# Kernel optimization log

Hardware: AMD Instinct MI355X
Metric: run time of the kernel (lower is better)

## Reference

```python
import jax, jax.numpy as jnp
import numpy as np

INPUT_DIM = 57
D_MODEL = 64
D_STATE = 16
D_CONV = 4
EXPAND = 2
N_LAYERS = 2
OUT_SIZE = 6
D_INNER = EXPAND * D_MODEL            # 128
DT_RANK = (D_MODEL + 15) // 16        # 4
BATCH, SEQ = 4, 4096


def setup_inputs() -> dict:
    key = jax.random.key(0)
    ks = jax.random.split(key, 12)
    s = 0.02
    nl = N_LAYERS
    x = jax.random.normal(ks[0], (BATCH, SEQ, INPUT_DIM), jnp.float32)
    w_in = jax.random.normal(ks[1], (D_MODEL, INPUT_DIM), jnp.float32) * s
    b_in = jnp.zeros((D_MODEL,), jnp.float32)
    in_proj_w = jax.random.normal(ks[2], (nl, 2 * D_INNER, D_MODEL), jnp.float32) * s
    conv_w = jax.random.normal(ks[3], (nl, D_INNER, 1, D_CONV), jnp.float32) * 0.2
    conv_b = jnp.zeros((nl, D_INNER), jnp.float32)
    x_proj_w = jax.random.normal(ks[4], (nl, DT_RANK + 2 * D_STATE, D_INNER), jnp.float32) * s
    dt_proj_w = jax.random.normal(ks[5], (nl, D_INNER, DT_RANK), jnp.float32) * 0.1
    dt_proj_b = jax.random.normal(ks[6], (nl, D_INNER), jnp.float32) * 0.1
    # S4D-real init: A[d, n] = n+1  ->  A_log = log(1..d_state)
    A_log = jnp.log(jnp.broadcast_to(
        jnp.arange(1, D_STATE + 1, dtype=jnp.float32)[None, None, :],
        (nl, D_INNER, D_STATE)))
    D_skip = jnp.ones((nl, D_INNER), jnp.float32)
    out_proj_w = jax.random.normal(ks[7], (nl, D_MODEL, D_INNER), jnp.float32) * s
    w_cls = jax.random.normal(ks[8], (OUT_SIZE, D_MODEL), jnp.float32) * s
    b_cls = jnp.zeros((OUT_SIZE,), jnp.float32)
    return {"x": x, "w_in": w_in, "b_in": b_in, "in_proj_w": in_proj_w,
            "conv_w": conv_w, "conv_b": conv_b, "x_proj_w": x_proj_w,
            "dt_proj_w": dt_proj_w, "dt_proj_b": dt_proj_b, "A_log": A_log,
            "D_skip": D_skip, "out_proj_w": out_proj_w,
            "w_cls": w_cls, "b_cls": b_cls}


def _mamba_block(h, ipw, cw, cb, xpw, dpw, dpb, Alog, Dp, opw):
    B, L, _ = h.shape
    xz = h @ ipw.T                                  # (B, L, 2*D_INNER)
    xp, z = jnp.split(xz, 2, axis=-1)
    # depthwise causal conv over time
    xc = jnp.transpose(xp, (0, 2, 1))               # (B, D_INNER, L)
    xc = jax.lax.conv_general_dilated(
        xc, cw, window_strides=(1,), padding=[(D_CONV - 1, 0)],
        dimension_numbers=("NCH", "OIH", "NCH"),
        feature_group_count=D_INNER) + cb[None, :, None]
    u = jax.nn.silu(jnp.transpose(xc, (0, 2, 1)))   # (B, L, D_INNER)
    dbl = u @ xpw.T                                 # (B, L, DT_RANK + 2*D_STATE)
    dt, Bm, Cm = jnp.split(dbl, [DT_RANK, DT_RANK + D_STATE], axis=-1)
    delta = jax.nn.softplus(dt @ dpw.T + dpb)       # (B, L, D_INNER)
    A = -jnp.exp(Alog)                              # (D_INNER, D_STATE)

    def step(hst, inp):
        u_t, d_t, B_t, C_t = inp                    # (B,Di), (B,Di), (B,N), (B,N)
        hst = jnp.exp(d_t[:, :, None] * A) * hst + \
              (d_t * u_t)[:, :, None] * B_t[:, None, :]
        y_t = jnp.einsum("bdn,bn->bd", hst, C_t)
        return hst, y_t

    h0 = jnp.zeros((B, D_INNER, D_STATE), h.dtype)
    xs = (jnp.swapaxes(u, 0, 1), jnp.swapaxes(delta, 0, 1),
          jnp.swapaxes(Bm, 0, 1), jnp.swapaxes(Cm, 0, 1))
    _, ys = jax.lax.scan(step, h0, xs)              # (L, B, D_INNER)
    y = jnp.swapaxes(ys, 0, 1) + u * Dp
    y = y * jax.nn.silu(z)
    return y @ opw.T                                # (B, L, D_MODEL)


def reference(x, w_in, b_in, in_proj_w, conv_w, conv_b, x_proj_w,
              dt_proj_w, dt_proj_b, A_log, D_skip, out_proj_w, w_cls, b_cls):
    h = x @ w_in.T + b_in                           # linear_in
    for i in range(N_LAYERS):                       # residual mamba blocks
        h = h + _mamba_block(h, in_proj_w[i], conv_w[i], conv_b[i],
                             x_proj_w[i], dt_proj_w[i], dt_proj_b[i],
                             A_log[i], D_skip[i], out_proj_w[i])
    pooled = jnp.mean(h, axis=1)                    # AdaptiveAvgPool1d(1)
    return pooled @ w_cls.T + b_cls
```

## Files before the change

kernel.cpp:

```cpp
#include <hip/hip_runtime.h>


#define NB 4
#define SL 4096
#define NC 256
#define CT 16

__device__ __forceinline__ float siluf(float x) { return x / (1.f + __expf(-x)); }
__device__ __forceinline__ float softplusf(float x) { return x > 20.f ? x : log1pf(__expf(x)); }

__global__ __launch_bounds__(256) void k_prep(const float* __restrict__ opw, float* __restrict__ opwT) {
  int i = blockIdx.x * 256 + threadIdx.x;
  int l = i >> 13;
  int rem = i & 8191;
  int d = rem >> 6, m = rem & 63;
  opwT[i] = opw[l * 8192 + m * 128 + d];
}

__global__ __launch_bounds__(256) void k_linin(const float* __restrict__ x, const float* __restrict__ w,
                                               const float* __restrict__ bias, float* __restrict__ h) {
  __shared__ __align__(16) float xs[64][60];
  __shared__ __align__(16) float ws[64][60];
  const int t = threadIdx.x;
  const int r0 = blockIdx.x * 64;
  for (int i = t; i < 64 * 57; i += 256) {
    int r = i / 57, k = i - r * 57;
    xs[r][k] = x[(r0 + r) * 57 + k];
    ws[r][k] = w[i];
  }
  for (int i = t; i < 64 * 3; i += 256) {
    int r = i / 3, j = i - r * 3;
    xs[r][57 + j] = 0.f;
    ws[r][57 + j] = 0.f;
  }
  __syncthreads();
  const int col = t & 63;
  const int rg = t >> 6;
  float wreg[15][4];
#pragma unroll
  for (int k4 = 0; k4 < 15; ++k4) {
    float4 v = *(const float4*)&ws[col][k4 * 4];
    wreg[k4][0] = v.x; wreg[k4][1] = v.y; wreg[k4][2] = v.z; wreg[k4][3] = v.w;
  }
  const float bcol = bias[col];
  for (int g = 0; g < 4; ++g) {
    const int rb = rg * 16 + g * 4;
    float acc[4] = {bcol, bcol, bcol, bcol};
#pragma unroll
    for (int k4 = 0; k4 < 15; ++k4) {
#pragma unroll
      for (int i = 0; i < 4; ++i) {
        float4 xv = *(const float4*)&xs[rb + i][k4 * 4];
        acc[i] = fmaf(xv.x, wreg[k4][0], acc[i]);
        acc[i] = fmaf(xv.y, wreg[k4][1], acc[i]);
        acc[i] = fmaf(xv.z, wreg[k4][2], acc[i]);
        acc[i] = fmaf(xv.w, wreg[k4][3], acc[i]);
      }
    }
#pragma unroll
    for (int i = 0; i < 4; ++i) h[(r0 + rb + i) * 64 + col] = acc[i];
  }
}

__global__ __launch_bounds__(256) void k_inproj(const float* __restrict__ hin, const float* __restrict__ W,
                                                float* __restrict__ xp, float* __restrict__ z) {
  __shared__ __align__(16) float ht[64][68];
  __shared__ __align__(16) float wt[64][68];
  const int t = threadIdx.x;
  const int r0 = blockIdx.x * 64;
  const int c0 = blockIdx.y * 64;
  for (int idx = t; idx < 64 * 16; idx += 256) {
    int r = idx >> 4, k4 = idx & 15;
    float4 v = *(const float4*)(hin + (r0 + r) * 64 + 4 * k4);
    ht[4 * k4 + 0][r] = v.x; ht[4 * k4 + 1][r] = v.y; ht[4 * k4 + 2][r] = v.z; ht[4 * k4 + 3][r] = v.w;
  }
  for (int idx = t; idx < 64 * 16; idx += 256) {
    int c = idx >> 4, k4 = idx & 15;
    float4 v = *(const float4*)(W + (c0 + c) * 64 + 4 * k4);
    wt[4 * k4 + 0][c] = v.x; wt[4 * k4 + 1][c] = v.y; wt[4 * k4 + 2][c] = v.z; wt[4 * k4 + 3][c] = v.w;
  }
  __syncthreads();
  const int tc = t & 15, tr = t >> 4;
  float acc[4][4] = {};
  for (int k = 0; k < 64; ++k) {
    float4 a = *(const float4*)&ht[k][4 * tr];
    float4 b = *(const float4*)&wt[k][4 * tc];
    float av[4] = {a.x, a.y, a.z, a.w};
    float bv[4] = {b.x, b.y, b.z, b.w};
#pragma unroll
    for (int i = 0; i < 4; ++i)
#pragma unroll
      for (int j = 0; j < 4; ++j) acc[i][j] = fmaf(av[i], bv[j], acc[i][j]);
  }
#pragma unroll
  for (int i = 0; i < 4; ++i) {
    int row = r0 + 4 * tr + i;
    int c = c0 + 4 * tc;
    float4 v = make_float4(acc[i][0], acc[i][1], acc[i][2], acc[i][3]);
    if (c0 < 128) *(float4*)(xp + row * 128 + c) = v;
    else          *(float4*)(z + row * 128 + (c - 128)) = v;
  }
}

__global__ __launch_bounds__(256, 4) void k_mid(const float* __restrict__ xp, const float* __restrict__ cw,
                                                const float* __restrict__ cb, const float* __restrict__ xpw,
                                                const float* __restrict__ dpw, const float* __restrict__ dpb,
                                                const float* __restrict__ Alog,
                                                float* __restrict__ u_g, float* __restrict__ dl_g,
                                                float* __restrict__ B_g, float* __restrict__ C_g,
                                                float* __restrict__ chP, float* __restrict__ chH) {
  __shared__ __align__(16) float ush[16][132];
  __shared__ __align__(16) float dsh[16][132];
  __shared__ __align__(16) float wsh[36][132];
  __shared__ __align__(16) float dbl[16][40];

  const int t = threadIdx.x;
  const int c = blockIdx.x;
  const int b = blockIdx.y;
  const int grow0 = b * SL + c * CT;

  for (int i = t; i < 36 * 128; i += 256) {
    int cc = i >> 7, dd = i & 127;
    wsh[cc][dd] = xpw[cc * 128 + dd];
  }
  for (int i = t; i < 16 * 128; i += 256) {
    int r = i >> 7, dd = i & 127;
    float4 cwv = *(const float4*)(cw + dd * 4);
    const float* base = xp + (size_t)(grow0 + r) * 128 + dd;
    int l = c * CT + r;
    float acc = cb[dd] + base[0] * cwv.w;
    if (l >= 1) acc += base[-128] * cwv.z;
    if (l >= 2) acc += base[-256] * cwv.y;
    if (l >= 3) acc += base[-384] * cwv.x;
    float uu = siluf(acc);
    ush[r][dd] = uu;
    u_g[(size_t)(grow0 + r) * 128 + dd] = uu;
  }
  __syncthreads();

  if (t < 144) {
    int r = t / 9, cg = t - (t / 9) * 9;
    int cc = cg * 4;
    float a0 = 0, a1 = 0, a2 = 0, a3 = 0;
#pragma unroll 8
    for (int k4 = 0; k4 < 32; ++k4) {
      float4 uu = *(const float4*)&ush[r][4 * k4];
      float4 w0 = *(const float4*)&wsh[cc + 0][4 * k4];
      float4 w1 = *(const float4*)&wsh[cc + 1][4 * k4];
      float4 w2 = *(const float4*)&wsh[cc + 2][4 * k4];
      float4 w3 = *(const float4*)&wsh[cc + 3][4 * k4];
      a0 += uu.x * w0.x + uu.y * w0.y + uu.z * w0.z + uu.w * w0.w;
      a1 += uu.x * w1.x + uu.y * w1.y + uu.z * w1.z + uu.w * w1.w;
      a2 += uu.x * w2.x + uu.y * w2.y + uu.z * w2.z + uu.w * w2.w;
      a3 += uu.x * w3.x + uu.y * w3.y + uu.z * w3.z + uu.w * w3.w;
    }
    dbl[r][cc + 0] = a0; dbl[r][cc + 1] = a1; dbl[r][cc + 2] = a2; dbl[r][cc + 3] = a3;
  }
  __syncthreads();

  for (int i = t; i < 16 * 128; i += 256) {
    int r = i >> 7, dd = i & 127;
    float4 wv = *(const float4*)(dpw + dd * 4);
    float acc = dpb[dd] + dbl[r][0] * wv.x + dbl[r][1] * wv.y + dbl[r][2] * wv.z + dbl[r][3] * wv.w;
    float dt = softplusf(acc);
    dsh[r][dd] = dt;
    dl_g[(size_t)(grow0 + r) * 128 + dd] = dt;
  }
  for (int i = t; i < 16 * 32; i += 256) {
    int r = i >> 5, j = i & 31;
    float v = dbl[r][4 + j];
    if (j < 16) B_g[(grow0 + r) * 16 + j] = v;
    else        C_g[(grow0 + r) * 16 + (j - 16)] = v;
  }
  __syncthreads();

  {
    const int d = t & 127, hf = t >> 7, n0 = hf * 8;
    float a[8], hst[8];
#pragma unroll
    for (int j = 0; j < 8; ++j) {
      a[j] = -__expf(Alog[d * 16 + n0 + j]);
      hst[j] = 0.f;
    }
    float dts = 0.f;
#pragma unroll 4
    for (int tt = 0; tt < CT; ++tt) {
      float dt = dsh[tt][d];
      float du = dt * ush[tt][d];
      dts += dt;
#pragma unroll
      for (int j = 0; j < 8; ++j) {
        float e = __expf(dt * a[j]);
        hst[j] = fmaf(e, hst[j], du * dbl[tt][4 + n0 + j]);
      }
    }
    int off = ((b * 128 + d) * NC + c) * 16 + n0;
    float p[8];
#pragma unroll
    for (int j = 0; j < 8; ++j) p[j] = __expf(dts * a[j]);
    *(float4*)(chP + off + 0) = make_float4(p[0], p[1], p[2], p[3]);
    *(float4*)(chP + off + 4) = make_float4(p[4], p[5], p[6], p[7]);
    *(float4*)(chH + off + 0) = make_float4(hst[0], hst[1], hst[2], hst[3]);
    *(float4*)(chH + off + 4) = make_float4(hst[4], hst[5], hst[6], hst[7]);
  }
}

__global__ __launch_bounds__(256) void k_scan2p(const float* __restrict__ chP, float* chH) {
  __shared__ float sP[16][16];
  __shared__ float sH[16][16];
  const int t = threadIdx.x;
  const int n = t & 15, g = t >> 4;
  const int d = blockIdx.x, b = blockIdx.y;
  const int base = ((b * 128 + d) * NC) * 16 + n;

  float Pl[16], Hl[16];
  float cp = 1.f, ch = 0.f;
#pragma unroll
  for (int i = 0; i < 16; ++i) {
    int idx = base + (g * 16 + i) * 16;
    float P = chP[idx];
    float H = chH[idx];
    Pl[i] = P; Hl[i] = H;
    ch = fmaf(P, ch, H);
    cp *= P;
  }
  sP[g][n] = cp; sH[g][n] = ch;
  __syncthreads();
#pragma unroll
  for (int s = 1; s < 16; s <<= 1) {
    float pL = 1.f, hL = 0.f;
    if (g >= s) { pL = sP[g - s][n]; hL = sH[g - s][n]; }
    __syncthreads();
    ch = fmaf(cp, hL, ch);
    cp = cp * pL;
    sP[g][n] = cp; sH[g][n] = ch;
    __syncthreads();
  }
  float carry = 0.f;
  if (g > 0) carry = sH[g - 1][n];
#pragma unroll
  for (int i = 0; i < 16; ++i) {
    int idx = base + (g * 16 + i) * 16;
    chH[idx] = carry;
    carry = fmaf(Pl[i], carry, Hl[i]);
  }
}

__global__ __launch_bounds__(256, 5) void k_back(const float* __restrict__ u_g, const float* __restrict__ dl_g,
                                                 const float* __restrict__ B_g, const float* __restrict__ C_g,
                                                 const float* __restrict__ z_g, const float* __restrict__ cin,
                                                 const float* __restrict__ Alog, const float* __restrict__ Dsk,
                                                 const float* __restrict__ opwT, float* __restrict__ h) {
  __shared__ __align__(16) float ush[16][132];
  __shared__ __align__(16) float dsh[16][132];
  __shared__ float bsh[16][16];
  __shared__ float csh[16][16];
  __shared__ __align__(16) float ygsh[128][20];

  const int t = threadIdx.x;
  const int c = blockIdx.x;
  const int b = blockIdx.y;
  const int grow0 = b * SL + c * CT;

  for (int i = t; i < 16 * 128; i += 256) {
    int r = i >> 7, dd = i & 127;
    ush[r][dd] = u_g[(size_t)(grow0 + r) * 128 + dd];
    dsh[r][dd] = dl_g[(size_t)(grow0 + r) * 128 + dd];
  }
  for (int i = t; i < 16 * 32; i += 256) {
    int r = i >> 5, j = i & 31;
    if (j < 16) bsh[r][j] = B_g[(grow0 + r) * 16 + j];
    else        csh[r][j - 16] = C_g[(grow0 + r) * 16 + (j - 16)];
  }
  __syncthreads();

  {
    const int d = t >> 1, hf = t & 1, n0 = hf * 8;
    float a[8], hst[8];
    size_t off = ((size_t)(b * 128 + d) * NC + c) * 16 + n0;
    float4 h0 = *(const float4*)(cin + off + 0);
    float4 h1 = *(const float4*)(cin + off + 4);
    hst[0] = h0.x; hst[1] = h0.y; hst[2] = h0.z; hst[3] = h0.w;
    hst[4] = h1.x; hst[5] = h1.y; hst[6] = h1.z; hst[7] = h1.w;
#pragma unroll
    for (int j = 0; j < 8; ++j) a[j] = -__expf(Alog[d * 16 + n0 + j]);
    const float Dd = Dsk[d];
#pragma unroll 4
    for (int tt = 0; tt < CT; ++tt) {
      float dt = dsh[tt][d];
      float ut = ush[tt][d];
      float du = dt * ut;
      float yv = 0.f;
#pragma unroll
      for (int j = 0; j < 8; ++j) {
        float e = __expf(dt * a[j]);
        hst[j] = fmaf(e, hst[j], du * bsh[tt][n0 + j]);
        yv = fmaf(hst[j], csh[tt][n0 + j], yv);
      }
      float tot = yv + __shfl_xor(yv, 1);
      if (hf == 0) {
        float y = tot + ut * Dd;
        float zv = z_g[(size_t)(grow0 + tt) * 128 + d];
        ygsh[d][tt] = y * siluf(zv);
      }
    }
  }
  __syncthreads();

  {
    const int o = t & 63, q = t >> 6;
    float acc0 = 0.f, acc1 = 0.f, acc2 = 0.f, acc3 = 0.f;
#pragma unroll 8
    for (int k = 0; k < 128; ++k) {
      float w = opwT[k * 64 + o];
      float4 yv = *(const float4*)&ygsh[k][q * 4];
      acc0 = fmaf(yv.x, w, acc0);
      acc1 = fmaf(yv.y, w, acc1);
      acc2 = fmaf(yv.z, w, acc2);
      acc3 = fmaf(yv.w, w, acc3);
    }
    h[(size_t)(grow0 + q * 4 + 0) * 64 + o] += acc0;
    h[(size_t)(grow0 + q * 4 + 1) * 64 + o] += acc1;
    h[(size_t)(grow0 + q * 4 + 2) * 64 + o] += acc2;
    h[(size_t)(grow0 + q * 4 + 3) * 64 + o] += acc3;
  }
}

__global__ __launch_bounds__(256) void k_poolpart(const float* __restrict__ h, float* __restrict__ pp) {
  const int lb = blockIdx.x;
  const int b = blockIdx.y;
  const int t = threadIdx.x;
  const int d = t & 63, part = t >> 6;
  float s = 0.f;
  for (int i = 0; i < 32; ++i) {
    int l = lb * 128 + part + i * 4;
    s += h[(size_t)(b * SL + l) * 64 + d];
  }
  __shared__ float red[256];
  red[t] = s;
  __syncthreads();
  if (t < 64) pp[(b * 32 + lb) * 64 + t] = red[t] + red[t + 64] + red[t + 128] + red[t + 192];
}

__global__ __launch_bounds__(256) void k_cls(const float* __restrict__ pp, const float* __restrict__ wc,
                                             const float* __restrict__ bc, float* __restrict__ out) {
  const int t = threadIdx.x;
  __shared__ float pooled[4][64];
  int b = t >> 6, d = t & 63;
  float s = 0.f;
  for (int lb = 0; lb < 32; ++lb) s += pp[(b * 32 + lb) * 64 + d];
  pooled[b][d] = s * (1.f / 4096.f);
  __syncthreads();
  if (t < 24) {
    int bb = t / 6, o = t - bb * 6;
    float acc = bc[o];
    for (int d2 = 0; d2 < 64; ++d2) acc += pooled[bb][d2] * wc[o * 64 + d2];
    out[bb * 6 + o] = acc;
  }
}

extern "C" void kernel_launch(void* const* d_in, const int* in_sizes, int n_in,
                              void* d_out, int out_size, void* d_ws, size_t ws_size,
                              hipStream_t stream) {
  const float* x    = (const float*)d_in[0];
  const float* w_in = (const float*)d_in[1];
  const float* b_in = (const float*)d_in[2];
  const float* ipw  = (const float*)d_in[3];
  const float* cw   = (const float*)d_in[4];
  const float* cb   = (const float*)d_in[5];
  const float* xpw  = (const float*)d_in[6];
  const float* dpw  = (const float*)d_in[7];
  const float* dpb  = (const float*)d_in[8];
  const float* Alog = (const float*)d_in[9];
  const float* Dsk  = (const float*)d_in[10];
  const float* opw  = (const float*)d_in[11];
  const float* wc   = (const float*)d_in[12];
  const float* bc   = (const float*)d_in[13];
  float* out = (float*)d_out;

  float* ws   = (float*)d_ws;
  float* h    = ws;
  float* xp   = h + 1048576;
  float* zb   = xp + 2097152;
  float* ub   = zb + 2097152;
  float* dl   = ub + 2097152;
  float* Bb   = dl + 2097152;
  float* Cb   = Bb + 262144;
  float* chP  = Cb + 262144;
  float* chH  = chP + 2097152;
  float* opwT = chH + 2097152;
  float* pp   = opwT + 16384;

  k_prep<<<64, 256, 0, stream>>>(opw, opwT);
  k_linin<<<256, 256, 0, stream>>>(x, w_in, b_in, h);
  for (int i = 0; i < 2; ++i) {
    k_inproj<<<dim3(256, 4), 256, 0, stream>>>(h, ipw + i * 16384, xp, zb);
    k_mid<<<dim3(NC, 4), 256, 0, stream>>>(xp, cw + i * 512, cb + i * 128,
                                           xpw + i * 4608, dpw + i * 512, dpb + i * 128,
                                           Alog + i * 2048, ub, dl, Bb, Cb, chP, chH);
    k_scan2p<<<dim3(128, 4), 256, 0, stream>>>(chP, chH);
    k_back<<<dim3(NC, 4), 256, 0, stream>>>(ub, dl, Bb, Cb, zb, chH,
                                            Alog + i * 2048, Dsk + i * 128,
                                            opwT + i * 8192, h);
  }
  k_poolpart<<<dim3(32, 4), 256, 0, stream>>>(h, pp);
  k_cls<<<1, 256, 0, stream>>>(pp, wc, bc, out);
}
```

Measured before the change: 246.7 us.

## Drop chunk decay buffer, fuse pooling into back kernel, remove prep kernels

k_mid now stores only the per-chunk dt sum instead of the full 16-state decay products. The scan kernel recomputes the decays from dt sum and A, and the chunk-state layout changes to chunk-major. Pooling moves into k_back through atomics on the last layer, which removes the poolpart kernel and the out_proj transpose prep kernel. The x_proj weights are read straight from global memory instead of being staged in LDS, and k_mid's occupancy hint is raised to 6. Atomics make the pooled sum order nondeterministic, and the scan's strided reads of dt sums may be less coalesced.

```diff
diff --git a/kernel.cpp b/kernel.cpp
--- a/kernel.cpp
+++ b/kernel.cpp
@@ -9,20 +9,14 @@
 __device__ __forceinline__ float siluf(float x) { return x / (1.f + __expf(-x)); }
 __device__ __forceinline__ float softplusf(float x) { return x > 20.f ? x : log1pf(__expf(x)); }
 
-__global__ __launch_bounds__(256) void k_prep(const float* __restrict__ opw, float* __restrict__ opwT) {
-  int i = blockIdx.x * 256 + threadIdx.x;
-  int l = i >> 13;
-  int rem = i & 8191;
-  int d = rem >> 6, m = rem & 63;
-  opwT[i] = opw[l * 8192 + m * 128 + d];
-}
-
 __global__ __launch_bounds__(256) void k_linin(const float* __restrict__ x, const float* __restrict__ w,
-                                               const float* __restrict__ bias, float* __restrict__ h) {
+                                               const float* __restrict__ bias, float* __restrict__ h,
+                                               float* __restrict__ pool) {
   __shared__ __align__(16) float xs[64][60];
   __shared__ __align__(16) float ws[64][60];
   const int t = threadIdx.x;
   const int r0 = blockIdx.x * 64;
+  if (blockIdx.x == 0) pool[t] = 0.f;
   for (int i = t; i < 64 * 57; i += 256) {
     int r = i / 57, k = i - r * 57;
     xs[r][k] = x[(r0 + r) * 57 + k];
@@ -102,16 +96,15 @@
   }
 }
 
-__global__ __launch_bounds__(256, 4) void k_mid(const float* __restrict__ xp, const float* __restrict__ cw,
+__global__ __launch_bounds__(256, 6) void k_mid(const float* __restrict__ xp, const float* __restrict__ cw,
                                                 const float* __restrict__ cb, const float* __restrict__ xpw,
                                                 const float* __restrict__ dpw, const float* __restrict__ dpb,
                                                 const float* __restrict__ Alog,
                                                 float* __restrict__ u_g, float* __restrict__ dl_g,
                                                 float* __restrict__ B_g, float* __restrict__ C_g,
-                                                float* __restrict__ chP, float* __restrict__ chH) {
+                                                float* __restrict__ chH, float* __restrict__ dtsumG) {
   __shared__ __align__(16) float ush[16][132];
   __shared__ __align__(16) float dsh[16][132];
-  __shared__ __align__(16) float wsh[36][132];
   __shared__ __align__(16) float dbl[16][40];
 
   const int t = threadIdx.x;
@@ -119,10 +112,6 @@
   const int b = blockIdx.y;
   const int grow0 = b * SL + c * CT;
 
-  for (int i = t; i < 36 * 128; i += 256) {
-    int cc = i >> 7, dd = i & 127;
-    wsh[cc][dd] = xpw[cc * 128 + dd];
-  }
   for (int i = t; i < 16 * 128; i += 256) {
     int r = i >> 7, dd = i & 127;
     float4 cwv = *(const float4*)(cw + dd * 4);
@@ -141,18 +130,19 @@
   if (t < 144) {
     int r = t / 9, cg = t - (t / 9) * 9;
     int cc = cg * 4;
+    const float4* w0 = (const float4*)(xpw + (cc + 0) * 128);
+    const float4* w1 = (const float4*)(xpw + (cc + 1) * 128);
+    const float4* w2 = (const float4*)(xpw + (cc + 2) * 128);
+    const float4* w3 = (const float4*)(xpw + (cc + 3) * 128);
     float a0 = 0, a1 = 0, a2 = 0, a3 = 0;
 #pragma unroll 8
     for (int k4 = 0; k4 < 32; ++k4) {
       float4 uu = *(const float4*)&ush[r][4 * k4];
-      float4 w0 = *(const float4*)&wsh[cc + 0][4 * k4];
-      float4 w1 = *(const float4*)&wsh[cc + 1][4 * k4];
-      float4 w2 = *(const float4*)&wsh[cc + 2][4 * k4];
-      float4 w3 = *(const float4*)&wsh[cc + 3][4 * k4];
-      a0 += uu.x * w0.x + uu.y * w0.y + uu.z * w0.z + uu.w * w0.w;
-      a1 += uu.x * w1.x + uu.y * w1.y + uu.z * w1.z + uu.w * w1.w;
-      a2 += uu.x * w2.x + uu.y * w2.y + uu.z * w2.z + uu.w * w2.w;
-      a3 += uu.x * w3.x + uu.y * w3.y + uu.z * w3.z + uu.w * w3.w;
+      float4 v0 = w0[k4], v1 = w1[k4], v2 = w2[k4], v3 = w3[k4];
+      a0 += uu.x * v0.x + uu.y * v0.y + uu.z * v0.z + uu.w * v0.w;
+      a1 += uu.x * v1.x + uu.y * v1.y + uu.z * v1.z + uu.w * v1.w;
+      a2 += uu.x * v2.x + uu.y * v2.y + uu.z * v2.z + uu.w * v2.w;
+      a3 += uu.x * v3.x + uu.y * v3.y + uu.z * v3.z + uu.w * v3.w;
     }
     dbl[r][cc + 0] = a0; dbl[r][cc + 1] = a1; dbl[r][cc + 2] = a2; dbl[r][cc + 3] = a3;
   }
@@ -194,35 +184,33 @@
         hst[j] = fmaf(e, hst[j], du * dbl[tt][4 + n0 + j]);
       }
     }
-    int off = ((b * 128 + d) * NC + c) * 16 + n0;
-    float p[8];
-#pragma unroll
-    for (int j = 0; j < 8; ++j) p[j] = __expf(dts * a[j]);
-    *(float4*)(chP + off + 0) = make_float4(p[0], p[1], p[2], p[3]);
-    *(float4*)(chP + off + 4) = make_float4(p[4], p[5], p[6], p[7]);
+    size_t off = ((size_t)(b * NC + c) * 128 + d) * 16 + n0;
     *(float4*)(chH + off + 0) = make_float4(hst[0], hst[1], hst[2], hst[3]);
     *(float4*)(chH + off + 4) = make_float4(hst[4], hst[5], hst[6], hst[7]);
-  }
-}
-
-__global__ __launch_bounds__(256) void k_scan2p(const float* __restrict__ chP, float* chH) {
+    if (hf == 0) dtsumG[(b * NC + c) * 128 + d] = dts;
+  }
+}
+
+__global__ __launch_bounds__(256) void k_scan2p(const float* __restrict__ Alog,
+                                                const float* __restrict__ dtsumG, float* chH) {
   __shared__ float sP[16][16];
   __shared__ float sH[16][16];
   const int t = threadIdx.x;
   const int n = t & 15, g = t >> 4;
   const int d = blockIdx.x, b = blockIdx.y;
-  const int base = ((b * 128 + d) * NC) * 16 + n;
-
-  float Pl[16], Hl[16];
+  const float A2 = -__expf(Alog[d * 16 + n]);
+
+  float el[16], Hl[16];
   float cp = 1.f, ch = 0.f;
 #pragma unroll
   for (int i = 0; i < 16; ++i) {
-    int idx = base + (g * 16 + i) * 16;
-    float P = chP[idx];
-    float H = chH[idx];
-    Pl[i] = P; Hl[i] = H;
-    ch = fmaf(P, ch, H);
-    cp *= P;
+    int cc = g * 16 + i;
+    float ds = dtsumG[(b * NC + cc) * 128 + d];
+    float e = __expf(ds * A2);
+    float H = chH[((size_t)(b * NC + cc) * 128 + d) * 16 + n];
+    el[i] = e; Hl[i] = H;
+    ch = fmaf(e, ch, H);
+    cp *= e;
   }
   sP[g][n] = cp; sH[g][n] = ch;
   __syncthreads();
@@ -240,9 +228,9 @@
   if (g > 0) carry = sH[g - 1][n];
 #pragma unroll
   for (int i = 0; i < 16; ++i) {
-    int idx = base + (g * 16 + i) * 16;
+    size_t idx = ((size_t)(b * NC + g * 16 + i) * 128 + d) * 16 + n;
     chH[idx] = carry;
-    carry = fmaf(Pl[i], carry, Hl[i]);
+    carry = fmaf(el[i], carry, Hl[i]);
   }
 }
 
@@ -250,7 +238,8 @@
                                                  const float* __restrict__ B_g, const float* __restrict__ C_g,
                                                  const float* __restrict__ z_g, const float* __restrict__ cin,
                                                  const float* __restrict__ Alog, const float* __restrict__ Dsk,
-                                                 const float* __restrict__ opwT, float* __restrict__ h) {
+                                                 const float* __restrict__ opw, float* __restrict__ h,
+                                                 float* __restrict__ pool, int doPool) {
   __shared__ __align__(16) float ush[16][132];
   __shared__ __align__(16) float dsh[16][132];
   __shared__ float bsh[16][16];
@@ -277,7 +266,7 @@
   {
     const int d = t >> 1, hf = t & 1, n0 = hf * 8;
     float a[8], hst[8];
-    size_t off = ((size_t)(b * 128 + d) * NC + c) * 16 + n0;
+    size_t off = ((size_t)(b * NC + c) * 128 + d) * 16 + n0;
     float4 h0 = *(const float4*)(cin + off + 0);
     float4 h1 = *(const float4*)(cin + off + 4);
     hst[0] = h0.x; hst[1] = h0.y; hst[2] = h0.z; hst[3] = h0.w;
@@ -311,51 +300,40 @@
     const int o = t & 63, q = t >> 6;
     float acc0 = 0.f, acc1 = 0.f, acc2 = 0.f, acc3 = 0.f;
 #pragma unroll 8
-    for (int k = 0; k < 128; ++k) {
-      float w = opwT[k * 64 + o];
-      float4 yv = *(const float4*)&ygsh[k][q * 4];
-      acc0 = fmaf(yv.x, w, acc0);
-      acc1 = fmaf(yv.y, w, acc1);
-      acc2 = fmaf(yv.z, w, acc2);
-      acc3 = fmaf(yv.w, w, acc3);
-    }
-    h[(size_t)(grow0 + q * 4 + 0) * 64 + o] += acc0;
-    h[(size_t)(grow0 + q * 4 + 1) * 64 + o] += acc1;
-    h[(size_t)(grow0 + q * 4 + 2) * 64 + o] += acc2;
-    h[(size_t)(grow0 + q * 4 + 3) * 64 + o] += acc3;
-  }
-}
-
-__global__ __launch_bounds__(256) void k_poolpart(const float* __restrict__ h, float* __restrict__ pp) {
-  const int lb = blockIdx.x;
-  const int b = blockIdx.y;
-  const int t = threadIdx.x;
-  const int d = t & 63, part = t >> 6;
-  float s = 0.f;
-  for (int i = 0; i < 32; ++i) {
-    int l = lb * 128 + part + i * 4;
-    s += h[(size_t)(b * SL + l) * 64 + d];
-  }
-  __shared__ float red[256];
-  red[t] = s;
-  __syncthreads();
-  if (t < 64) pp[(b * 32 + lb) * 64 + t] = red[t] + red[t + 64] + red[t + 128] + red[t + 192];
-}
-
-__global__ __launch_bounds__(256) void k_cls(const float* __restrict__ pp, const float* __restrict__ wc,
-                                             const float* __restrict__ bc, float* __restrict__ out) {
-  const int t = threadIdx.x;
-  __shared__ float pooled[4][64];
-  int b = t >> 6, d = t & 63;
-  float s = 0.f;
-  for (int lb = 0; lb < 32; ++lb) s += pp[(b * 32 + lb) * 64 + d];
-  pooled[b][d] = s * (1.f / 4096.f);
-  __syncthreads();
+    for (int k4 = 0; k4 < 32; ++k4) {
+      float4 w4 = *(const float4*)(opw + o * 128 + 4 * k4);
+      float4 y0 = *(const float4*)&ygsh[4 * k4 + 0][q * 4];
+      float4 y1 = *(const float4*)&ygsh[4 * k4 + 1][q * 4];
+      float4 y2 = *(const float4*)&ygsh[4 * k4 + 2][q * 4];
+      float4 y3 = *(const float4*)&ygsh[4 * k4 + 3][q * 4];
+      acc0 = fmaf(y0.x, w4.x, acc0); acc0 = fmaf(y1.x, w4.y, acc0);
+      acc0 = fmaf(y2.x, w4.z, acc0); acc0 = fmaf(y3.x, w4.w, acc0);
+      acc1 = fmaf(y0.y, w4.x, acc1); acc1 = fmaf(y1.y, w4.y, acc1);
+      acc1 = fmaf(y2.y, w4.z, acc1); acc1 = fmaf(y3.y, w4.w, acc1);
+      acc2 = fmaf(y0.z, w4.x, acc2); acc2 = fmaf(y1.z, w4.y, acc2);
+      acc2 = fmaf(y2.z, w4.z, acc2); acc2 = fmaf(y3.z, w4.w, acc2);
+      acc3 = fmaf(y0.w, w4.x, acc3); acc3 = fmaf(y1.w, w4.y, acc3);
+      acc3 = fmaf(y2.w, w4.z, acc3); acc3 = fmaf(y3.w, w4.w, acc3);
+    }
+    size_t row = (size_t)(grow0 + q * 4) * 64 + o;
+    float h0 = h[row + 0 * 64] + acc0;
+    float h1 = h[row + 1 * 64] + acc1;
+    float h2 = h[row + 2 * 64] + acc2;
+    float h3 = h[row + 3 * 64] + acc3;
+    h[row + 0 * 64] = h0; h[row + 1 * 64] = h1;
+    h[row + 2 * 64] = h2; h[row + 3 * 64] = h3;
+    if (doPool) atomicAdd(pool + b * 64 + o, h0 + h1 + h2 + h3);
+  }
+}
+
+__global__ __launch_bounds__(64) void k_cls(const float* __restrict__ pool, const float* __restrict__ wc,
+                                            const float* __restrict__ bc, float* __restrict__ out) {
+  const int t = threadIdx.x;
   if (t < 24) {
     int bb = t / 6, o = t - bb * 6;
-    float acc = bc[o];
-    for (int d2 = 0; d2 < 64; ++d2) acc += pooled[bb][d2] * wc[o * 64 + d2];
-    out[bb * 6 + o] = acc;
+    float acc = 0.f;
+    for (int d2 = 0; d2 < 64; ++d2) acc += pool[bb * 64 + d2] * wc[o * 64 + d2];
+    out[bb * 6 + o] = bc[o] + acc * (1.f / 4096.f);
   }
 }
 
@@ -378,31 +356,28 @@
   const float* bc   = (const float*)d_in[13];
   float* out = (float*)d_out;
 
-  float* ws   = (float*)d_ws;
-  float* h    = ws;
-  float* xp   = h + 1048576;
-  float* zb   = xp + 2097152;
-  float* ub   = zb + 2097152;
-  float* dl   = ub + 2097152;
-  float* Bb   = dl + 2097152;
-  float* Cb   = Bb + 262144;
-  float* chP  = Cb + 262144;
-  float* chH  = chP + 2097152;
-  float* opwT = chH + 2097152;
-  float* pp   = opwT + 16384;
-
-  k_prep<<<64, 256, 0, stream>>>(opw, opwT);
-  k_linin<<<256, 256, 0, stream>>>(x, w_in, b_in, h);
+  float* ws    = (float*)d_ws;
+  float* h     = ws;
+  float* xp    = h + 1048576;
+  float* zb    = xp + 2097152;
+  float* ub    = zb + 2097152;
+  float* dl    = ub + 2097152;
+  float* Bb    = dl + 2097152;
+  float* Cb    = Bb + 262144;
+  float* chH   = Cb + 262144;
+  float* dtsum = chH + 2097152;
+  float* pool  = dtsum + 131072;
+
+  k_linin<<<256, 256, 0, stream>>>(x, w_in, b_in, h, pool);
   for (int i = 0; i < 2; ++i) {
     k_inproj<<<dim3(256, 4), 256, 0, stream>>>(h, ipw + i * 16384, xp, zb);
     k_mid<<<dim3(NC, 4), 256, 0, stream>>>(xp, cw + i * 512, cb + i * 128,
                                            xpw + i * 4608, dpw + i * 512, dpb + i * 128,
-                                           Alog + i * 2048, ub, dl, Bb, Cb, chP, chH);
-    k_scan2p<<<dim3(128, 4), 256, 0, stream>>>(chP, chH);
+                                           Alog + i * 2048, ub, dl, Bb, Cb, chH, dtsum);
+    k_scan2p<<<dim3(128, 4), 256, 0, stream>>>(Alog + i * 2048, dtsum, chH);
     k_back<<<dim3(NC, 4), 256, 0, stream>>>(ub, dl, Bb, Cb, zb, chH,
                                             Alog + i * 2048, Dsk + i * 128,
-                                            opwT + i * 8192, h);
-  }
-  k_poolpart<<<dim3(32, 4), 256, 0, stream>>>(h, pp);
-  k_cls<<<1, 256, 0, stream>>>(pp, wc, bc, out);
-}
+                                            opw + i * 8192, h, pool, i == 1 ? 1 : 0);
+  }
+  k_cls<<<1, 64, 0, stream>>>(pool, wc, bc, out);
+}
```

Measured after the change: 342.1 us. +38.7%, slower.
